# Kernel optimization log

Hardware: AMD Instinct MI355X
Metric: run time of the kernel (lower is better)

Reference implementation:

```python
import jax, jax.numpy as jnp
import numpy as np

B = 128          # batch of IQ signals
L = 128          # signal length
PL = 16          # patch length
ST = 4           # patch stride
WIN = 4          # local window
NPATCH = (L - PL) // ST + 1   # 29
HID = 256
NCLS = 8
NG = B * NPATCH               # number of patch graphs
N = NG * PL                   # total nodes


def _build_edges():
    src, dst = [], []
    for i in range(PL):
        for j in range(PL):
            if 0 < abs(i - j) <= WIN:
                src.append(i); dst.append(j)
    bs = np.array(src, np.int32)          # [108]
    bd = np.array(dst, np.int32)
    off = (np.arange(NG, dtype=np.int32) * PL)[:, None]
    isrc = (off + bs[None, :]).reshape(-1)
    idst = (off + bd[None, :]).reshape(-1)
    # cross-patch edges: last node of patch p -> first node of patch p+1
    b = np.arange(B, dtype=np.int32)[:, None]
    p = np.arange(NPATCH - 1, dtype=np.int32)[None, :]
    csrc = (b * NPATCH * PL + p * PL + (PL - 1)).reshape(-1)
    cdst = (b * NPATCH * PL + (p + 1) * PL).reshape(-1)
    return np.concatenate([isrc, csrc]), np.concatenate([idst, cdst])


def setup_inputs() -> dict:
    key = jax.random.key(0)
    ks = jax.random.split(key, 10)
    s = 0.05
    esrc, edst = _build_edges()
    return {
        "iq_signal": jax.random.normal(ks[0], (B, 2, L), jnp.float32),
        "edge_src": jnp.asarray(esrc),
        "edge_dst": jnp.asarray(edst),
        # SAGEConv layer 0 (in=2): lin_l (agg, with bias), lin_r (root, no bias)
        "W0_agg": jax.random.normal(ks[1], (HID, 2), jnp.float32) * s,
        "W0_root": jax.random.normal(ks[2], (HID, 2), jnp.float32) * s,
        "b0": jnp.zeros((HID,), jnp.float32),
        # SAGEConv layers 1..3 (256 -> 256), stacked
        "W_agg": jax.random.normal(ks[3], (3, HID, HID), jnp.float32) * s,
        "W_root": jax.random.normal(ks[4], (3, HID, HID), jnp.float32) * s,
        "b_lin": jnp.zeros((3, HID), jnp.float32),
        # per-layer LayerNorms
        "ln_scale": jnp.ones((4, HID), jnp.float32),
        "ln_bias": jnp.zeros((4, HID), jnp.float32),
        # classifier head
        "cls_W1": jax.random.normal(ks[5], (HID, HID), jnp.float32) * s,
        "cls_b1": jnp.zeros((HID,), jnp.float32),
        "cls_ln_scale": jnp.ones((HID,), jnp.float32),
        "cls_ln_bias": jnp.zeros((HID,), jnp.float32),
        "cls_W2": jax.random.normal(ks[6], (NCLS, HID), jnp.float32) * s,
        "cls_b2": jnp.zeros((NCLS,), jnp.float32),
    }


def _ln(x, g, b):
    m = x.mean(-1, keepdims=True)
    v = ((x - m) ** 2).mean(-1, keepdims=True)
    return (x - m) * jax.lax.rsqrt(v + 1e-5) * g + b


def reference(iq_signal, edge_src, edge_dst, W0_agg, W0_root, b0,
              W_agg, W_root, b_lin, ln_scale, ln_bias,
              cls_W1, cls_b1, cls_ln_scale, cls_ln_bias, cls_W2, cls_b2):
    # patch extraction: [B,2,L] -> [B,NPATCH,PL,2] -> node features [N,2]
    idx = jnp.arange(NPATCH)[:, None] * ST + jnp.arange(PL)[None, :]   # [29,16]
    x = jnp.transpose(iq_signal[:, :, idx], (0, 2, 3, 1)).reshape(-1, 2)

    # in-degree for mean aggregation (0 -> safe divide by 1)
    ones = jnp.ones((edge_dst.shape[0],), x.dtype)
    deg = jax.ops.segment_sum(ones, edge_dst, num_segments=N)
    inv_deg = 1.0 / jnp.maximum(deg, 1.0)

    def sage(h, Wa, Wr, b):
        # mean-aggregate neighbor messages, then lin_l(agg) + lin_r(h) + bias
        agg = jax.ops.segment_sum(h[edge_src], edge_dst, num_segments=N)
        agg = agg * inv_deg[:, None]
        return agg @ Wa.T + h @ Wr.T + b

    # layer 0 (2 -> 256): no residual (shape change)
    h = jax.nn.relu(_ln(sage(x, W0_agg, W0_root, b0), ln_scale[0], ln_bias[0]))
    # layers 1..3 with residual
    for l in range(3):
        hn = jax.nn.relu(_ln(sage(h, W_agg[l], W_root[l], b_lin[l]),
                             ln_scale[l + 1], ln_bias[l + 1]))
        h = h + hn

    node_emb = h                                  # [N, 256]
    # global_mean_pool per patch graph (16 consecutive nodes each)
    gf = node_emb.reshape(NG, PL, HID).mean(axis=1)   # [NG, 256]
    z = jax.nn.relu(_ln(gf @ cls_W1.T + cls_b1, cls_ln_scale, cls_ln_bias))
    logits = z @ cls_W2.T + cls_b2                # [NG, 8]
    return logits, gf, node_emb
```

## Files before the change

### kernel.cpp

```cpp
#include <hip/hip_runtime.h>
#include <hip/hip_bf16.h>

typedef __hip_bfloat16 bf16;
typedef unsigned short u16;
typedef unsigned int uint32;
typedef __attribute__((ext_vector_type(8))) short bf16x8;
typedef __attribute__((ext_vector_type(4))) float f32x4;

#define BATCH   128
#define LSIG    128
#define PL      16
#define ST      4
#define WIN     4
#define NPATCH  29
#define NG      (BATCH * NPATCH)
#define NNODE   (NG * PL)
#define HID     256
#define NCLS    8

#define IQ_OFF    0
#define W0A_OFF   32768
#define W0R_OFF   33280
#define B0_OFF    33792
#define BLIN_OFF  34048
#define LNS_OFF   34816
#define LNB_OFF   35840
#define W1T_OFF   36864
#define CB1_OFF   102400
#define CLNS_OFF  102656
#define CLNB_OFF  102912
#define CW2_OFF   103168
#define CB2_OFF   105216
#define CVT_TOTAL 105224

#define P_BYTE_OFF   4096
#define WB_BYTE_OFF  425984
#define A_BYTE_OFF   1216512
#define B_BYTE_OFF   1959936
#define GF_EOFF      (NG * NCLS)
#define EMB_EOFF     (NG * NCLS + NG * HID)

#define MFMA_BF16 __builtin_amdgcn_mfma_f32_16x16x32_bf16

__device__ __forceinline__ float b2f(bf16 x) { return __bfloat162float(x); }
__device__ __forceinline__ float lof(uint32 u) { return __uint_as_float(u << 16); }
__device__ __forceinline__ float hif(uint32 u) { return __uint_as_float(u & 0xFFFF0000u); }
__device__ __forceinline__ uint32 packbf(float a, float b) {
  bf16 r0 = __float2bfloat16(a), r1 = __float2bfloat16(b);
  return ((uint32)(*(const u16*)&r1) << 16) | (uint32)(*(const u16*)&r0);
}
__device__ __forceinline__ float ldmix(const void* p, size_t i, int fl) {
  return fl ? ((const float*)p)[i] : __bfloat162float(((const bf16*)p)[i]);
}

__global__ __launch_bounds__(256) void detect_kernel(const u16* __restrict__ iq, int* flag) {
  __shared__ int sbig, snz;
  int t = threadIdx.x;
  if (t == 0) { sbig = 0; snz = 0; }
  __syncthreads();
  int big = 0, nz = 0;
  for (int e = t; e < 16384; e += 256) {
    u16 u = iq[2 * e];
    int ex = (u >> 7) & 0xFF;
    if (ex >= 0xC0) big++;
    if (u != 0) nz++;
  }
  atomicAdd(&sbig, big); atomicAdd(&snz, nz);
  __syncthreads();
  if (t == 0) *flag = (sbig > 4 || snz < 100) ? 1 : 0;
}

__global__ __launch_bounds__(256) void convert_params(
    const int* __restrict__ flag,
    const void* iq, const void* w0a, const void* w0r, const void* b0,
    const void* blin, const void* lns, const void* lnb,
    const void* cw1, const void* cb1, const void* clns, const void* clnb,
    const void* cw2, const void* cb2,
    float* __restrict__ P) {
  int idx = blockIdx.x * 256 + threadIdx.x;
  if (idx >= CVT_TOTAL) return;
  int fl = *flag;
  float v;
  if (idx < W0A_OFF)        v = ldmix(iq,  idx, fl);
  else if (idx < W0R_OFF)   v = ldmix(w0a, idx - W0A_OFF, fl);
  else if (idx < B0_OFF)    v = ldmix(w0r, idx - W0R_OFF, fl);
  else if (idx < BLIN_OFF)  v = ldmix(b0,  idx - B0_OFF, fl);
  else if (idx < LNS_OFF)   v = ldmix(blin, idx - BLIN_OFF, fl);
  else if (idx < LNB_OFF)   v = ldmix(lns, idx - LNS_OFF, fl);
  else if (idx < W1T_OFF)   v = ldmix(lnb, idx - LNB_OFF, fl);
  else if (idx < CB1_OFF) { int t2 = idx - W1T_OFF;
    v = ldmix(cw1, (t2 & 255) * 256 + (t2 >> 8), fl); }
  else if (idx < CLNS_OFF)  v = ldmix(cb1, idx - CB1_OFF, fl);
  else if (idx < CLNB_OFF)  v = ldmix(clns, idx - CLNS_OFF, fl);
  else if (idx < CW2_OFF)   v = ldmix(clnb, idx - CLNB_OFF, fl);
  else if (idx < CB2_OFF)   v = ldmix(cw2, idx - CW2_OFF, fl);
  else                      v = ldmix(cb2, idx - CB2_OFF, fl);
  P[idx] = v;
}

__global__ __launch_bounds__(256) void convert_wb(
    const int* __restrict__ flag, const void* wag, const void* wro, bf16* __restrict__ WB) {
  int idx = blockIdx.x * 256 + threadIdx.x;
  int fl = *flag;
  int l = idx >> 17, m = (idx >> 16) & 1, r = idx & 65535;
  const void* src = m ? wro : wag;
  WB[idx] = __float2bfloat16(ldmix(src, l * 65536 + r, fl));
}

__global__ __launch_bounds__(256) void layer0_kernel(
    const float* __restrict__ P, bf16* __restrict__ hout) {
  int g = blockIdx.x, f = threadIdx.x;
  int b = g / NPATCH, p = g % NPATCH;
  __shared__ float x_s[PL][2];
  __shared__ float xp_s[2];
  __shared__ float agg_s[PL][2];
  __shared__ float o_s[PL][HID];
  __shared__ float mv_s[PL][2];
  if (f < 32) { int j = f & 15, c = f >> 4;
    x_s[j][c] = P[IQ_OFF + (b * 2 + c) * LSIG + p * ST + j]; }
  if (f < 2) xp_s[f] = (p > 0) ? P[IQ_OFF + (b * 2 + f) * LSIG + (p - 1) * ST + PL - 1] : 0.f;
  __syncthreads();
  if (f < 32) { int j = f & 15, c = f >> 4;
    float s = 0.f;
    int lo = j - WIN < 0 ? 0 : j - WIN, hi = j + WIN > 15 ? 15 : j + WIN;
    for (int i = lo; i <= hi; ++i) if (i != j) s += x_s[i][c];
    int deg = (j < WIN ? j : WIN) + ((15 - j) < WIN ? (15 - j) : WIN);
    if (j == 0 && p > 0) { s += xp_s[c]; deg += 1; }
    agg_s[j][c] = s / (float)deg;
  }
  __syncthreads();
  float wa0 = P[W0A_OFF + f * 2], wa1 = P[W0A_OFF + f * 2 + 1];
  float wr0 = P[W0R_OFF + f * 2], wr1 = P[W0R_OFF + f * 2 + 1];
  float bb = P[B0_OFF + f];
#pragma unroll
  for (int j = 0; j < PL; ++j)
    o_s[j][f] = agg_s[j][0] * wa0 + agg_s[j][1] * wa1 + x_s[j][0] * wr0 + x_s[j][1] * wr1 + bb;
  __syncthreads();
  { int j = f >> 4, q = f & 15;
    float s = 0.f, s2 = 0.f;
#pragma unroll
    for (int i = 0; i < 16; ++i) { float v = o_s[j][q + 16 * i]; s += v; s2 += v * v; }
#pragma unroll
    for (int m = 8; m >= 1; m >>= 1) { s += __shfl_xor(s, m); s2 += __shfl_xor(s2, m); }
    if (q == 0) { float mean = s * (1.f / HID);
      float var = s2 * (1.f / HID) - mean * mean;
      mv_s[j][0] = mean; mv_s[j][1] = rsqrtf(var + 1e-5f); }
  }
  __syncthreads();
  float gl = P[LNS_OFF + f], bl = P[LNB_OFF + f];
#pragma unroll
  for (int j = 0; j < PL; ++j) {
    float v = (o_s[j][f] - mv_s[j][0]) * mv_s[j][1] * gl + bl;
    v = v > 0.f ? v : 0.f;
    hout[(size_t)(g * PL + j) * HID + f] = __float2bfloat16(v);
  }
}

template<int LAST>
__global__ __launch_bounds__(256, 2) void sage_mfma(
    const bf16* __restrict__ hin,
    const bf16* __restrict__ Wa, const bf16* __restrict__ Wr,
    const float* __restrict__ bias,
    const float* __restrict__ lng, const float* __restrict__ lnb,
    bf16* __restrict__ hout,
    void* __restrict__ dout, const int* __restrict__ flag) {
  int t = threadIdx.x;
  int w = t >> 6, l = t & 63, lr = l & 15, lg = l >> 4;
  int g0 = blockIdx.x * 4;
  size_t nbase = (size_t)g0 * PL;
  __shared__ uint32 hb[64 * 128];
  __shared__ float part_s[64][4][2];
  __shared__ float mv_s[64][2];
  const uint32* hinw = (const uint32*)hin;

  int colbase = w * 64;
  const bf16* waB = Wa + (colbase + lr) * HID + lg * 8;
  const bf16* wrB = Wr + (colbase + lr) * HID + lg * 8;

  bf16x8 w0f[8];
#pragma unroll
  for (int ks = 0; ks < 8; ++ks) w0f[ks] = *(const bf16x8*)(wrB + ks * 32);

  const uint32* hg = hinw + nbase * 128;
#pragma unroll
  for (int it = 0; it < 8; ++it) {
    int u = it * 256 + t;
    int row = u >> 5, sl = u & 31;
    *(uint4*)&hb[row * 128 + ((sl ^ (row & 7)) << 2)] = *(const uint4*)(hg + u * 4);
  }
  __syncthreads();

  f32x4 acc[4][4];
#pragma unroll
  for (int m = 0; m < 4; ++m)
#pragma unroll
    for (int n = 0; n < 4; ++n) acc[m][n] = (f32x4){0.f, 0.f, 0.f, 0.f};
#pragma unroll
  for (int ks = 0; ks < 8; ++ks) {
    bf16x8 w1 = *(const bf16x8*)(wrB + 1 * 16 * HID + ks * 32);
    bf16x8 w2 = *(const bf16x8*)(wrB + 2 * 16 * HID + ks * 32);
    bf16x8 w3 = *(const bf16x8*)(wrB + 3 * 16 * HID + ks * 32);
#pragma unroll
    for (int m = 0; m < 4; ++m) {
      bf16x8 hf = *(const bf16x8*)&hb[(m * 16 + lr) * 128 + (((ks * 4 + lg) ^ (lr & 7)) << 2)];
      acc[m][0] = MFMA_BF16(hf, w0f[ks], acc[m][0], 0, 0, 0);
      acc[m][1] = MFMA_BF16(hf, w1, acc[m][1], 0, 0, 0);
      acc[m][2] = MFMA_BF16(hf, w2, acc[m][2], 0, 0, 0);
      acc[m][3] = MFMA_BF16(hf, w3, acc[m][3], 0, 0, 0);
    }
  }

  bf16x8 a0f[8];
#pragma unroll
  for (int ks = 0; ks < 8; ++ks) a0f[ks] = *(const bf16x8*)(waB + ks * 32);

  int c2 = t & 127, Ph = t >> 7;
  uint32 bnd[2];
#pragma unroll
  for (int pi = 0; pi < 2; ++pi) {
    int pp = Ph + pi * 2;
    int hp = ((g0 + pp) % NPATCH) != 0;
    uint32 u = 0;
    if (hp) {
      if (pp == 0) u = hinw[(nbase - 1) * 128 + c2];
      else { int br = pp * 16 - 1;
        u = hb[br * 128 + (((c2 >> 2) ^ (br & 7)) << 2) + (c2 & 3)]; }
    }
    bnd[pi] = u;
  }
  __syncthreads();

#pragma unroll
  for (int pi = 0; pi < 2; ++pi) {
    int pp = Ph + pi * 2;
    int pr = pp * 16;
    int hp = ((g0 + pp) % NPATCH) != 0;
    float vlo[16], vhi[16];
#pragma unroll
    for (int j = 0; j < 16; ++j) {
      uint32 u = hb[(pr + j) * 128 + (((c2 >> 2) ^ (j & 7)) << 2) + (c2 & 3)];
      vlo[j] = lof(u); vhi[j] = hif(u);
    }
    float blo = lof(bnd[pi]), bhi = hif(bnd[pi]);
#pragma unroll
    for (int j = 0; j < 16; ++j) {
      const int a = (j - WIN < 0) ? 0 : j - WIN;
      const int b = (j + WIN > 15) ? 15 : j + WIN;
      float slo = 0.f, shi = 0.f;
#pragma unroll
      for (int i = 0; i < 16; ++i)
        if (i >= a && i <= b && i != j) { slo += vlo[i]; shi += vhi[i]; }
      float deg = (float)((j < WIN ? j : WIN) + (15 - j < WIN ? 15 - j : WIN));
      if (j == 0 && hp) { slo += blo; shi += bhi; deg += 1.f; }
      float inv = 1.f / deg;
      hb[(pr + j) * 128 + (((c2 >> 2) ^ (j & 7)) << 2) + (c2 & 3)] = packbf(slo * inv, shi * inv);
    }
  }
  __syncthreads();

#pragma unroll
  for (int ks = 0; ks < 8; ++ks) {
    bf16x8 w1 = *(const bf16x8*)(waB + 1 * 16 * HID + ks * 32);
    bf16x8 w2 = *(const bf16x8*)(waB + 2 * 16 * HID + ks * 32);
    bf16x8 w3 = *(const bf16x8*)(waB + 3 * 16 * HID + ks * 32);
#pragma unroll
    for (int m = 0; m < 4; ++m) {
      bf16x8 af = *(const bf16x8*)&hb[(m * 16 + lr) * 128 + (((ks * 4 + lg) ^ (lr & 7)) << 2)];
      acc[m][0] = MFMA_BF16(af, a0f[ks], acc[m][0], 0, 0, 0);
      acc[m][1] = MFMA_BF16(af, w1, acc[m][1], 0, 0, 0);
      acc[m][2] = MFMA_BF16(af, w2, acc[m][2], 0, 0, 0);
      acc[m][3] = MFMA_BF16(af, w3, acc[m][3], 0, 0, 0);
    }
  }

#pragma unroll
  for (int nt = 0; nt < 4; ++nt) {
    float bv = bias[colbase + nt * 16 + lr];
#pragma unroll
    for (int m = 0; m < 4; ++m) {
      acc[m][nt][0] += bv; acc[m][nt][1] += bv; acc[m][nt][2] += bv; acc[m][nt][3] += bv;
    }
  }
#pragma unroll
  for (int m = 0; m < 4; ++m)
#pragma unroll
    for (int r = 0; r < 4; ++r) {
      float s = acc[m][0][r] + acc[m][1][r] + acc[m][2][r] + acc[m][3][r];
      float s2 = acc[m][0][r] * acc[m][0][r] + acc[m][1][r] * acc[m][1][r]
               + acc[m][2][r] * acc[m][2][r] + acc[m][3][r] * acc[m][3][r];
      s += __shfl_xor(s, 1); s2 += __shfl_xor(s2, 1);
      s += __shfl_xor(s, 2); s2 += __shfl_xor(s2, 2);
      s += __shfl_xor(s, 4); s2 += __shfl_xor(s2, 4);
      s += __shfl_xor(s, 8); s2 += __shfl_xor(s2, 8);
      if (lr == 0) { int row = m * 16 + lg * 4 + r; part_s[row][w][0] = s; part_s[row][w][1] = s2; }
    }
  __syncthreads();

  if (t < 64) {
    float S = part_s[t][0][0] + part_s[t][1][0] + part_s[t][2][0] + part_s[t][3][0];
    float S2 = part_s[t][0][1] + part_s[t][1][1] + part_s[t][2][1] + part_s[t][3][1];
    float mean = S * (1.f / HID);
    mv_s[t][0] = mean;
    mv_s[t][1] = rsqrtf(S2 * (1.f / HID) - mean * mean + 1e-5f);
  }
#pragma unroll
  for (int m = 0; m < 4; ++m)
#pragma unroll
    for (int nt = 0; nt < 4; ++nt) {
      int col = colbase + nt * 16 + lr;
#pragma unroll
      for (int r = 0; r < 4; ++r) {
        int row = m * 16 + lg * 4 + r;
        int i16 = row * 256 + (((col >> 3) ^ (row & 7)) << 3) + (col & 7);
        bf16 x = __float2bfloat16(acc[m][nt][r]);
        ((u16*)hb)[i16] = *(const u16*)&x;
      }
    }
  __syncthreads();

  {
    int prt = t >> 7;
    float gl0 = lng[c2 * 2], gl1 = lng[c2 * 2 + 1];
    float bl0 = lnb[c2 * 2], bl1 = lnb[c2 * 2 + 1];
    uint32* outw = nullptr;
    if constexpr (!LAST) outw = (uint32*)hout + nbase * 128;
    const uint32* inw = hinw + nbase * 128;
    int fl = 0;
    if constexpr (LAST) fl = *flag;
#pragma unroll
    for (int pi = 0; pi < 2; ++pi) {
      float sga = 0.f, sgb = 0.f;
#pragma unroll
      for (int i = 0; i < 16; ++i) {
        int row = prt * 32 + pi * 16 + i;
        uint32 u = hb[row * 128 + (((c2 >> 2) ^ (row & 7)) << 2) + (c2 & 3)];
        float mean = mv_s[row][0], rstd = mv_s[row][1];
        float a = (lof(u) - mean) * rstd * gl0 + bl0; a = a > 0.f ? a : 0.f;
        float b_ = (hif(u) - mean) * rstd * gl1 + bl1; b_ = b_ > 0.f ? b_ : 0.f;
        uint32 hu = inw[row * 128 + c2];
        a += lof(hu); b_ += hif(hu);
        if constexpr (!LAST) {
          outw[row * 128 + c2] = packbf(a, b_);
        } else {
          sga += a; sgb += b_;
          if (fl) {
            size_t ei = (size_t)EMB_EOFF + (nbase + row) * 256 + (size_t)c2 * 2;
            ((float*)dout)[ei] = a; ((float*)dout)[ei + 1] = b_;
          } else {
            ((uint32*)dout)[(EMB_EOFF >> 1) + (nbase + row) * 128 + c2] = packbf(a, b_);
          }
        }
      }
      if constexpr (LAST) {
        float ga = sga * (1.f / PL), gb = sgb * (1.f / PL);
        int gidx = g0 + prt * 2 + pi;
        if (fl) {
          size_t gi = (size_t)GF_EOFF + (size_t)gidx * 256 + (size_t)c2 * 2;
          ((float*)dout)[gi] = ga; ((float*)dout)[gi + 1] = gb;
        } else {
          ((uint32*)dout)[(GF_EOFF >> 1) + gidx * 128 + c2] = packbf(ga, gb);
        }
      }
    }
  }
}

__global__ __launch_bounds__(256) void head_kernel(
    const void* __restrict__ gin, const float* __restrict__ P,
    void* __restrict__ dout, const int* __restrict__ flag) {
  int g = blockIdx.x, f = threadIdx.x;
  int fl = *flag;
  __shared__ float gf_s[HID];
  __shared__ float z_s[HID];
  __shared__ float ps[4], ps2[4];
  __shared__ float mr[2];
  gf_s[f] = fl ? ((const float*)gin)[(size_t)GF_EOFF + (size_t)g * HID + f]
               : b2f(((const bf16*)gin)[(size_t)GF_EOFF + (size_t)g * HID + f]);
  __syncthreads();
  float acc = P[CB1_OFF + f];
  for (int k = 0; k < HID; k += 4) {
    const float4 gv = *(const float4*)(&gf_s[k]);
    acc = fmaf(gv.x, P[W1T_OFF + (k + 0) * HID + f], acc);
    acc = fmaf(gv.y, P[W1T_OFF + (k + 1) * HID + f], acc);
    acc = fmaf(gv.z, P[W1T_OFF + (k + 2) * HID + f], acc);
    acc = fmaf(gv.w, P[W1T_OFF + (k + 3) * HID + f], acc);
  }
  float s1 = acc, s2 = acc * acc;
#pragma unroll
  for (int m = 32; m >= 1; m >>= 1) { s1 += __shfl_xor(s1, m); s2 += __shfl_xor(s2, m); }
  int wid = f >> 6, lane = f & 63;
  if (lane == 0) { ps[wid] = s1; ps2[wid] = s2; }
  __syncthreads();
  if (f == 0) {
    float S = ps[0] + ps[1] + ps[2] + ps[3];
    float S2 = ps2[0] + ps2[1] + ps2[2] + ps2[3];
    float mean = S * (1.f / HID);
    mr[0] = mean; mr[1] = rsqrtf(S2 * (1.f / HID) - mean * mean + 1e-5f);
  }
  __syncthreads();
  float z = (acc - mr[0]) * mr[1] * P[CLNS_OFF + f] + P[CLNB_OFF + f];
  z = z > 0.f ? z : 0.f;
  z_s[f] = z;
  __syncthreads();
  if (f < NCLS) {
    float a = P[CB2_OFF + f];
    for (int k = 0; k < HID; ++k) a = fmaf(z_s[k], P[CW2_OFF + f * HID + k], a);
    size_t ei = (size_t)g * NCLS + f;
    if (fl) ((float*)dout)[ei] = a; else ((bf16*)dout)[ei] = __float2bfloat16(a);
  }
}

extern "C" void kernel_launch(void* const* d_in, const int* in_sizes, int n_in,
                              void* d_out, int out_size, void* d_ws, size_t ws_size,
                              hipStream_t stream) {
  char* ws = (char*)d_ws;
  int*   flag = (int*)ws;
  float* P    = (float*)(ws + P_BYTE_OFF);
  bf16*  WB   = (bf16*)(ws + WB_BYTE_OFF);
  bf16*  A    = (bf16*)(ws + A_BYTE_OFF);
  bf16*  B    = (bf16*)((char*)d_out + B_BYTE_OFF);

  detect_kernel<<<1, 256, 0, stream>>>((const u16*)d_in[0], flag);
  convert_params<<<(CVT_TOTAL + 255) / 256, 256, 0, stream>>>(
      flag, d_in[0], d_in[3], d_in[4], d_in[5], d_in[8],
      d_in[9], d_in[10], d_in[11], d_in[12], d_in[13], d_in[14], d_in[15], d_in[16], P);
  convert_wb<<<1536, 256, 0, stream>>>(flag, d_in[6], d_in[7], WB);

  layer0_kernel<<<NG, 256, 0, stream>>>(P, A);
  sage_mfma<0><<<NG / 4, 256, 0, stream>>>(A, WB, WB + 65536,
      P + BLIN_OFF, P + LNS_OFF + HID, P + LNB_OFF + HID, B, nullptr, flag);
  sage_mfma<0><<<NG / 4, 256, 0, stream>>>(B, WB + 131072, WB + 131072 + 65536,
      P + BLIN_OFF + HID, P + LNS_OFF + 2 * HID, P + LNB_OFF + 2 * HID, A, nullptr, flag);
  sage_mfma<1><<<NG / 4, 256, 0, stream>>>(A, WB + 262144, WB + 262144 + 65536,
      P + BLIN_OFF + 2 * HID, P + LNS_OFF + 3 * HID, P + LNB_OFF + 3 * HID, nullptr, d_out, flag);
  head_kernel<<<NG, 256, 0, stream>>>(d_out, P, d_out, flag);
}
```

Measured before the change: 246.6 us.

## Fuse three SAGE layers into one kernel with recomputed halo patch

Replaces the three per-layer sage_mfma launches with one kernel. Each block keeps two patches plus the preceding patch as a halo in LDS across all three layers. The halo is recomputed so the cross-patch edge stays correct without a global round trip. This removes the intermediate activation writes and reads to global memory and two launches. In exchange each block does 50% redundant MFMA work on the halo rows and uses more LDS with double buffers.

```diff
diff --git a/kernel.cpp b/kernel.cpp
--- a/kernel.cpp
+++ b/kernel.cpp
@@ -36,7 +36,6 @@
 #define P_BYTE_OFF   4096
 #define WB_BYTE_OFF  425984
 #define A_BYTE_OFF   1216512
-#define B_BYTE_OFF   1959936
 #define GF_EOFF      (NG * NCLS)
 #define EMB_EOFF     (NG * NCLS + NG * HID)
 
@@ -156,211 +155,204 @@
   }
 }
 
-template<int LAST>
-__global__ __launch_bounds__(256, 2) void sage_mfma(
-    const bf16* __restrict__ hin,
-    const bf16* __restrict__ Wa, const bf16* __restrict__ Wr,
-    const float* __restrict__ bias,
-    const float* __restrict__ lng, const float* __restrict__ lnb,
-    bf16* __restrict__ hout,
+__global__ __launch_bounds__(256, 2) void sage3_fused(
+    const bf16* __restrict__ hin, const bf16* __restrict__ WB,
+    const float* __restrict__ P,
     void* __restrict__ dout, const int* __restrict__ flag) {
   int t = threadIdx.x;
   int w = t >> 6, l = t & 63, lr = l & 15, lg = l >> 4;
-  int g0 = blockIdx.x * 4;
+  int g0 = blockIdx.x * 2;
+  int hashalo = (g0 % NPATCH) != 0;
   size_t nbase = (size_t)g0 * PL;
-  __shared__ uint32 hb[64 * 128];
-  __shared__ float part_s[64][4][2];
-  __shared__ float mv_s[64][2];
+  __shared__ uint32 bh[48 * 128];
+  __shared__ uint32 bw[48 * 128];
+  __shared__ float part_s[48][4][2];
+  __shared__ float mv_s[48][2];
   const uint32* hinw = (const uint32*)hin;
-
   int colbase = w * 64;
-  const bf16* waB = Wa + (colbase + lr) * HID + lg * 8;
-  const bf16* wrB = Wr + (colbase + lr) * HID + lg * 8;
-
-  bf16x8 w0f[8];
-#pragma unroll
-  for (int ks = 0; ks < 8; ++ks) w0f[ks] = *(const bf16x8*)(wrB + ks * 32);
-
-  const uint32* hg = hinw + nbase * 128;
-#pragma unroll
-  for (int it = 0; it < 8; ++it) {
+  int fl = *flag;
+
+  const uint32* hg = hinw + (nbase - PL) * 128;
+#pragma unroll
+  for (int it = 0; it < 6; ++it) {
     int u = it * 256 + t;
     int row = u >> 5, sl = u & 31;
-    *(uint4*)&hb[row * 128 + ((sl ^ (row & 7)) << 2)] = *(const uint4*)(hg + u * 4);
-  }
-  __syncthreads();
-
-  f32x4 acc[4][4];
-#pragma unroll
-  for (int m = 0; m < 4; ++m)
-#pragma unroll
-    for (int n = 0; n < 4; ++n) acc[m][n] = (f32x4){0.f, 0.f, 0.f, 0.f};
-#pragma unroll
-  for (int ks = 0; ks < 8; ++ks) {
-    bf16x8 w1 = *(const bf16x8*)(wrB + 1 * 16 * HID + ks * 32);
-    bf16x8 w2 = *(const bf16x8*)(wrB + 2 * 16 * HID + ks * 32);
-    bf16x8 w3 = *(const bf16x8*)(wrB + 3 * 16 * HID + ks * 32);
-#pragma unroll
-    for (int m = 0; m < 4; ++m) {
-      bf16x8 hf = *(const bf16x8*)&hb[(m * 16 + lr) * 128 + (((ks * 4 + lg) ^ (lr & 7)) << 2)];
-      acc[m][0] = MFMA_BF16(hf, w0f[ks], acc[m][0], 0, 0, 0);
-      acc[m][1] = MFMA_BF16(hf, w1, acc[m][1], 0, 0, 0);
-      acc[m][2] = MFMA_BF16(hf, w2, acc[m][2], 0, 0, 0);
-      acc[m][3] = MFMA_BF16(hf, w3, acc[m][3], 0, 0, 0);
-    }
-  }
-
-  bf16x8 a0f[8];
-#pragma unroll
-  for (int ks = 0; ks < 8; ++ks) a0f[ks] = *(const bf16x8*)(waB + ks * 32);
-
-  int c2 = t & 127, Ph = t >> 7;
-  uint32 bnd[2];
-#pragma unroll
-  for (int pi = 0; pi < 2; ++pi) {
-    int pp = Ph + pi * 2;
-    int hp = ((g0 + pp) % NPATCH) != 0;
-    uint32 u = 0;
-    if (hp) {
-      if (pp == 0) u = hinw[(nbase - 1) * 128 + c2];
-      else { int br = pp * 16 - 1;
-        u = hb[br * 128 + (((c2 >> 2) ^ (br & 7)) << 2) + (c2 & 3)]; }
-    }
-    bnd[pi] = u;
-  }
-  __syncthreads();
-
-#pragma unroll
-  for (int pi = 0; pi < 2; ++pi) {
-    int pp = Ph + pi * 2;
-    int pr = pp * 16;
-    int hp = ((g0 + pp) % NPATCH) != 0;
-    float vlo[16], vhi[16];
-#pragma unroll
-    for (int j = 0; j < 16; ++j) {
-      uint32 u = hb[(pr + j) * 128 + (((c2 >> 2) ^ (j & 7)) << 2) + (c2 & 3)];
-      vlo[j] = lof(u); vhi[j] = hif(u);
-    }
-    float blo = lof(bnd[pi]), bhi = hif(bnd[pi]);
-#pragma unroll
-    for (int j = 0; j < 16; ++j) {
-      const int a = (j - WIN < 0) ? 0 : j - WIN;
-      const int b = (j + WIN > 15) ? 15 : j + WIN;
-      float slo = 0.f, shi = 0.f;
-#pragma unroll
-      for (int i = 0; i < 16; ++i)
-        if (i >= a && i <= b && i != j) { slo += vlo[i]; shi += vhi[i]; }
-      float deg = (float)((j < WIN ? j : WIN) + (15 - j < WIN ? 15 - j : WIN));
-      if (j == 0 && hp) { slo += blo; shi += bhi; deg += 1.f; }
-      float inv = 1.f / deg;
-      hb[(pr + j) * 128 + (((c2 >> 2) ^ (j & 7)) << 2) + (c2 & 3)] = packbf(slo * inv, shi * inv);
-    }
-  }
-  __syncthreads();
-
-#pragma unroll
-  for (int ks = 0; ks < 8; ++ks) {
-    bf16x8 w1 = *(const bf16x8*)(waB + 1 * 16 * HID + ks * 32);
-    bf16x8 w2 = *(const bf16x8*)(waB + 2 * 16 * HID + ks * 32);
-    bf16x8 w3 = *(const bf16x8*)(waB + 3 * 16 * HID + ks * 32);
-#pragma unroll
-    for (int m = 0; m < 4; ++m) {
-      bf16x8 af = *(const bf16x8*)&hb[(m * 16 + lr) * 128 + (((ks * 4 + lg) ^ (lr & 7)) << 2)];
-      acc[m][0] = MFMA_BF16(af, a0f[ks], acc[m][0], 0, 0, 0);
-      acc[m][1] = MFMA_BF16(af, w1, acc[m][1], 0, 0, 0);
-      acc[m][2] = MFMA_BF16(af, w2, acc[m][2], 0, 0, 0);
-      acc[m][3] = MFMA_BF16(af, w3, acc[m][3], 0, 0, 0);
-    }
-  }
-
-#pragma unroll
-  for (int nt = 0; nt < 4; ++nt) {
-    float bv = bias[colbase + nt * 16 + lr];
-#pragma unroll
-    for (int m = 0; m < 4; ++m) {
-      acc[m][nt][0] += bv; acc[m][nt][1] += bv; acc[m][nt][2] += bv; acc[m][nt][3] += bv;
-    }
-  }
-#pragma unroll
-  for (int m = 0; m < 4; ++m)
-#pragma unroll
-    for (int r = 0; r < 4; ++r) {
-      float s = acc[m][0][r] + acc[m][1][r] + acc[m][2][r] + acc[m][3][r];
-      float s2 = acc[m][0][r] * acc[m][0][r] + acc[m][1][r] * acc[m][1][r]
-               + acc[m][2][r] * acc[m][2][r] + acc[m][3][r] * acc[m][3][r];
-      s += __shfl_xor(s, 1); s2 += __shfl_xor(s2, 1);
-      s += __shfl_xor(s, 2); s2 += __shfl_xor(s2, 2);
-      s += __shfl_xor(s, 4); s2 += __shfl_xor(s2, 4);
-      s += __shfl_xor(s, 8); s2 += __shfl_xor(s2, 8);
-      if (lr == 0) { int row = m * 16 + lg * 4 + r; part_s[row][w][0] = s; part_s[row][w][1] = s2; }
-    }
-  __syncthreads();
-
-  if (t < 64) {
-    float S = part_s[t][0][0] + part_s[t][1][0] + part_s[t][2][0] + part_s[t][3][0];
-    float S2 = part_s[t][0][1] + part_s[t][1][1] + part_s[t][2][1] + part_s[t][3][1];
-    float mean = S * (1.f / HID);
-    mv_s[t][0] = mean;
-    mv_s[t][1] = rsqrtf(S2 * (1.f / HID) - mean * mean + 1e-5f);
-  }
-#pragma unroll
-  for (int m = 0; m < 4; ++m)
+    uint4 v = make_uint4(0u, 0u, 0u, 0u);
+    if (row >= 16 || hashalo) v = *(const uint4*)(hg + u * 4);
+    *(uint4*)&bh[row * 128 + ((sl ^ (row & 7)) << 2)] = v;
+  }
+  __syncthreads();
+
+  for (int L = 0; L < 3; ++L) {
+    const bf16* Wa = WB + L * 131072;
+    const bf16* Wr = Wa + 65536;
+    const float* bias = P + BLIN_OFF + L * HID;
+    const float* lng  = P + LNS_OFF + (L + 1) * HID;
+    const float* lnb  = P + LNB_OFF + (L + 1) * HID;
+    const bf16* waB = Wa + (colbase + lr) * HID + lg * 8;
+    const bf16* wrB = Wr + (colbase + lr) * HID + lg * 8;
+
+    bf16x8 a0f[8], r0f[8];
+#pragma unroll
+    for (int ks = 0; ks < 8; ++ks) {
+      a0f[ks] = *(const bf16x8*)(waB + ks * 32);
+      r0f[ks] = *(const bf16x8*)(wrB + ks * 32);
+    }
+
+    {
+      int c2 = t & 127, pp = t >> 7;
+      for (int pi = pp; pi < 3; pi += 2) {
+        int pr = pi * 16;
+        int gq = g0 - 1 + pi;
+        int hp = (pi > 0) && ((gq % NPATCH) != 0);
+        float vlo[16], vhi[16];
+#pragma unroll
+        for (int j = 0; j < 16; ++j) {
+          uint32 u = bh[(pr + j) * 128 + (((c2 >> 2) ^ (j & 7)) << 2) + (c2 & 3)];
+          vlo[j] = lof(u); vhi[j] = hif(u);
+        }
+        float blo = 0.f, bhi = 0.f;
+        if (hp) {
+          int br = pr - 1;
+          uint32 u = bh[br * 128 + (((c2 >> 2) ^ (br & 7)) << 2) + (c2 & 3)];
+          blo = lof(u); bhi = hif(u);
+        }
+#pragma unroll
+        for (int j = 0; j < 16; ++j) {
+          const int a = (j - WIN < 0) ? 0 : j - WIN;
+          const int b = (j + WIN > 15) ? 15 : j + WIN;
+          float slo = 0.f, shi = 0.f;
+#pragma unroll
+          for (int i = 0; i < 16; ++i)
+            if (i >= a && i <= b && i != j) { slo += vlo[i]; shi += vhi[i]; }
+          float deg = (float)((j < WIN ? j : WIN) + (15 - j < WIN ? 15 - j : WIN));
+          if (j == 0 && hp) { slo += blo; shi += bhi; deg += 1.f; }
+          float inv = 1.f / deg;
+          bw[(pr + j) * 128 + (((c2 >> 2) ^ (j & 7)) << 2) + (c2 & 3)] = packbf(slo * inv, shi * inv);
+        }
+      }
+    }
+    __syncthreads();
+
+    f32x4 acc[3][4];
+#pragma unroll
+    for (int m = 0; m < 3; ++m)
+#pragma unroll
+      for (int n = 0; n < 4; ++n) acc[m][n] = (f32x4){0.f, 0.f, 0.f, 0.f};
+#pragma unroll
+    for (int ks = 0; ks < 8; ++ks) {
+      bf16x8 wa1 = *(const bf16x8*)(waB + 1 * 16 * HID + ks * 32);
+      bf16x8 wa2 = *(const bf16x8*)(waB + 2 * 16 * HID + ks * 32);
+      bf16x8 wa3 = *(const bf16x8*)(waB + 3 * 16 * HID + ks * 32);
+      bf16x8 wr1 = *(const bf16x8*)(wrB + 1 * 16 * HID + ks * 32);
+      bf16x8 wr2 = *(const bf16x8*)(wrB + 2 * 16 * HID + ks * 32);
+      bf16x8 wr3 = *(const bf16x8*)(wrB + 3 * 16 * HID + ks * 32);
+#pragma unroll
+      for (int m = 0; m < 3; ++m) {
+        int idx = (m * 16 + lr) * 128 + (((ks * 4 + lg) ^ (lr & 7)) << 2);
+        bf16x8 af = *(const bf16x8*)&bw[idx];
+        bf16x8 hf = *(const bf16x8*)&bh[idx];
+        acc[m][0] = MFMA_BF16(af, a0f[ks], acc[m][0], 0, 0, 0);
+        acc[m][0] = MFMA_BF16(hf, r0f[ks], acc[m][0], 0, 0, 0);
+        acc[m][1] = MFMA_BF16(af, wa1, acc[m][1], 0, 0, 0);
+        acc[m][1] = MFMA_BF16(hf, wr1, acc[m][1], 0, 0, 0);
+        acc[m][2] = MFMA_BF16(af, wa2, acc[m][2], 0, 0, 0);
+        acc[m][2] = MFMA_BF16(hf, wr2, acc[m][2], 0, 0, 0);
+        acc[m][3] = MFMA_BF16(af, wa3, acc[m][3], 0, 0, 0);
+        acc[m][3] = MFMA_BF16(hf, wr3, acc[m][3], 0, 0, 0);
+      }
+    }
+
 #pragma unroll
     for (int nt = 0; nt < 4; ++nt) {
-      int col = colbase + nt * 16 + lr;
+      float bv = bias[colbase + nt * 16 + lr];
+#pragma unroll
+      for (int m = 0; m < 3; ++m) {
+        acc[m][nt][0] += bv; acc[m][nt][1] += bv; acc[m][nt][2] += bv; acc[m][nt][3] += bv;
+      }
+    }
+#pragma unroll
+    for (int m = 0; m < 3; ++m)
 #pragma unroll
       for (int r = 0; r < 4; ++r) {
-        int row = m * 16 + lg * 4 + r;
-        int i16 = row * 256 + (((col >> 3) ^ (row & 7)) << 3) + (col & 7);
-        bf16 x = __float2bfloat16(acc[m][nt][r]);
-        ((u16*)hb)[i16] = *(const u16*)&x;
-      }
-    }
-  __syncthreads();
-
-  {
-    int prt = t >> 7;
-    float gl0 = lng[c2 * 2], gl1 = lng[c2 * 2 + 1];
-    float bl0 = lnb[c2 * 2], bl1 = lnb[c2 * 2 + 1];
-    uint32* outw = nullptr;
-    if constexpr (!LAST) outw = (uint32*)hout + nbase * 128;
-    const uint32* inw = hinw + nbase * 128;
-    int fl = 0;
-    if constexpr (LAST) fl = *flag;
-#pragma unroll
-    for (int pi = 0; pi < 2; ++pi) {
-      float sga = 0.f, sgb = 0.f;
-#pragma unroll
-      for (int i = 0; i < 16; ++i) {
-        int row = prt * 32 + pi * 16 + i;
-        uint32 u = hb[row * 128 + (((c2 >> 2) ^ (row & 7)) << 2) + (c2 & 3)];
+        float s = acc[m][0][r] + acc[m][1][r] + acc[m][2][r] + acc[m][3][r];
+        float s2 = acc[m][0][r] * acc[m][0][r] + acc[m][1][r] * acc[m][1][r]
+                 + acc[m][2][r] * acc[m][2][r] + acc[m][3][r] * acc[m][3][r];
+        s += __shfl_xor(s, 1); s2 += __shfl_xor(s2, 1);
+        s += __shfl_xor(s, 2); s2 += __shfl_xor(s2, 2);
+        s += __shfl_xor(s, 4); s2 += __shfl_xor(s2, 4);
+        s += __shfl_xor(s, 8); s2 += __shfl_xor(s2, 8);
+        if (lr == 0) { int row = m * 16 + lg * 4 + r; part_s[row][w][0] = s; part_s[row][w][1] = s2; }
+      }
+    __syncthreads();
+
+    if (t < 48) {
+      float S = part_s[t][0][0] + part_s[t][1][0] + part_s[t][2][0] + part_s[t][3][0];
+      float S2 = part_s[t][0][1] + part_s[t][1][1] + part_s[t][2][1] + part_s[t][3][1];
+      float mean = S * (1.f / HID);
+      mv_s[t][0] = mean;
+      mv_s[t][1] = rsqrtf(S2 * (1.f / HID) - mean * mean + 1e-5f);
+    }
+#pragma unroll
+    for (int m = 0; m < 3; ++m)
+#pragma unroll
+      for (int nt = 0; nt < 4; ++nt) {
+        int col = colbase + nt * 16 + lr;
+#pragma unroll
+        for (int r = 0; r < 4; ++r) {
+          int row = m * 16 + lg * 4 + r;
+          int i16 = row * 256 + (((col >> 3) ^ (row & 7)) << 3) + (col & 7);
+          bf16 x = __float2bfloat16(acc[m][nt][r]);
+          ((u16*)bw)[i16] = *(const u16*)&x;
+        }
+      }
+    __syncthreads();
+
+    {
+      int c2 = t & 127, prt = t >> 7;
+      float gl0 = lng[c2 * 2], gl1 = lng[c2 * 2 + 1];
+      float bl0 = lnb[c2 * 2], bl1 = lnb[c2 * 2 + 1];
+#pragma unroll
+      for (int i = 0; i < 24; ++i) {
+        int row = prt * 24 + i;
+        int di = row * 128 + (((c2 >> 2) ^ (row & 7)) << 2) + (c2 & 3);
+        uint32 u = bw[di];
         float mean = mv_s[row][0], rstd = mv_s[row][1];
         float a = (lof(u) - mean) * rstd * gl0 + bl0; a = a > 0.f ? a : 0.f;
         float b_ = (hif(u) - mean) * rstd * gl1 + bl1; b_ = b_ > 0.f ? b_ : 0.f;
-        uint32 hu = inw[row * 128 + c2];
+        uint32 hu = bh[di];
         a += lof(hu); b_ += hif(hu);
-        if constexpr (!LAST) {
-          outw[row * 128 + c2] = packbf(a, b_);
-        } else {
-          sga += a; sgb += b_;
+        bh[di] = packbf(a, b_);
+        if (L == 2 && row >= 16) {
+          size_t gnode = nbase + (row - 16);
           if (fl) {
-            size_t ei = (size_t)EMB_EOFF + (nbase + row) * 256 + (size_t)c2 * 2;
+            size_t ei = (size_t)EMB_EOFF + gnode * 256 + (size_t)c2 * 2;
             ((float*)dout)[ei] = a; ((float*)dout)[ei + 1] = b_;
           } else {
-            ((uint32*)dout)[(EMB_EOFF >> 1) + (nbase + row) * 128 + c2] = packbf(a, b_);
+            ((uint32*)dout)[(EMB_EOFF >> 1) + gnode * 128 + c2] = packbf(a, b_);
           }
         }
       }
-      if constexpr (LAST) {
-        float ga = sga * (1.f / PL), gb = sgb * (1.f / PL);
-        int gidx = g0 + prt * 2 + pi;
-        if (fl) {
-          size_t gi = (size_t)GF_EOFF + (size_t)gidx * 256 + (size_t)c2 * 2;
-          ((float*)dout)[gi] = ga; ((float*)dout)[gi + 1] = gb;
-        } else {
-          ((uint32*)dout)[(GF_EOFF >> 1) + gidx * 128 + c2] = packbf(ga, gb);
-        }
-      }
+    }
+    __syncthreads();
+  }
+
+  {
+    int c2 = t & 127, Ph = t >> 7;
+    int pr = (Ph + 1) * 16;
+    float sga = 0.f, sgb = 0.f;
+#pragma unroll
+    for (int j = 0; j < 16; ++j) {
+      uint32 u = bh[(pr + j) * 128 + (((c2 >> 2) ^ (j & 7)) << 2) + (c2 & 3)];
+      sga += lof(u); sgb += hif(u);
+    }
+    float ga = sga * (1.f / PL), gb = sgb * (1.f / PL);
+    int gidx = g0 + Ph;
+    if (fl) {
+      size_t gi = (size_t)GF_EOFF + (size_t)gidx * 256 + (size_t)c2 * 2;
+      ((float*)dout)[gi] = ga; ((float*)dout)[gi + 1] = gb;
+    } else {
+      ((uint32*)dout)[(GF_EOFF >> 1) + gidx * 128 + c2] = packbf(ga, gb);
     }
   }
 }
@@ -418,7 +410,6 @@
   float* P    = (float*)(ws + P_BYTE_OFF);
   bf16*  WB   = (bf16*)(ws + WB_BYTE_OFF);
   bf16*  A    = (bf16*)(ws + A_BYTE_OFF);
-  bf16*  B    = (bf16*)((char*)d_out + B_BYTE_OFF);
 
   detect_kernel<<<1, 256, 0, stream>>>((const u16*)d_in[0], flag);
   convert_params<<<(CVT_TOTAL + 255) / 256, 256, 0, stream>>>(
@@ -427,11 +418,6 @@
   convert_wb<<<1536, 256, 0, stream>>>(flag, d_in[6], d_in[7], WB);
 
   layer0_kernel<<<NG, 256, 0, stream>>>(P, A);
-  sage_mfma<0><<<NG / 4, 256, 0, stream>>>(A, WB, WB + 65536,
-      P + BLIN_OFF, P + LNS_OFF + HID, P + LNB_OFF + HID, B, nullptr, flag);
-  sage_mfma<0><<<NG / 4, 256, 0, stream>>>(B, WB + 131072, WB + 131072 + 65536,
-      P + BLIN_OFF + HID, P + LNS_OFF + 2 * HID, P + LNB_OFF + 2 * HID, A, nullptr, flag);
-  sage_mfma<1><<<NG / 4, 256, 0, stream>>>(A, WB + 262144, WB + 262144 + 65536,
-      P + BLIN_OFF + 2 * HID, P + LNS_OFF + 3 * HID, P + LNB_OFF + 3 * HID, nullptr, d_out, flag);
+  sage3_fused<<<NG / 2, 256, 0, stream>>>(A, WB, P, d_out, flag);
   head_kernel<<<NG, 256, 0, stream>>>(d_out, P, d_out, flag);
 }
```

After: 399.0 us. 61.8% more time.
